# Optimization experiments

Hardware: AMD Instinct MI355X
Metric: run time of the kernel (lower is better)

Reference implementation:

```python
import jax, jax.numpy as jnp
import numpy as np
from jax import lax

DN = ('NCHW', 'OIHW', 'NCHW')

def _conv(x, k, stride):
    return lax.conv_general_dilated(x, k, (stride, stride), 'VALID', dimension_numbers=DN)

def setup_inputs() -> dict:
    key = jax.random.key(0)
    ks = jax.random.split(key, 20)
    B, E, A, D = 2048, 8, 6, 64 * 7 * 7  # batch, rm_states, actions, flat conv dim (3136)
    s = 0.05
    inp = {
        'state': jax.random.normal(ks[0], (B, 84, 84, 3), jnp.float32),
        'rm_state': jax.random.randint(ks[1], (B,), 0, E, jnp.int64),
        # conv encoder params
        'k1': jax.random.normal(ks[2], (32, 3, 8, 8), jnp.float32) * s,
        'c1': jnp.zeros((32,), jnp.float32),
        'k2': jax.random.normal(ks[3], (64, 32, 4, 4), jnp.float32) * s,
        'c2': jnp.zeros((64,), jnp.float32),
        'k3': jax.random.normal(ks[4], (64, 64, 3, 3), jnp.float32) * s,
        'c3': jnp.zeros((64,), jnp.float32),
        # stacked per-rm-state expert MLP params (E experts)
        'W1': jax.random.normal(ks[5], (E, D, 64), jnp.float32) * s,
        'B1': jnp.zeros((E, 64), jnp.float32),
        'W2': jax.random.normal(ks[6], (E, 64, 64), jnp.float32) * s,
        'B2': jnp.zeros((E, 64), jnp.float32),
        'W3': jax.random.normal(ks[7], (E, 64, 64), jnp.float32) * s,
        'B3': jnp.zeros((E, 64), jnp.float32),
        'W4': jax.random.normal(ks[8], (E, 64, 64), jnp.float32) * s,
        'B4': jnp.zeros((E, 64), jnp.float32),
        'W5': jax.random.normal(ks[9], (E, 64, 64), jnp.float32) * s,
        'B5': jnp.zeros((E, 64), jnp.float32),
        'W6': jax.random.normal(ks[10], (E, 64, A), jnp.float32) * s,
        'B6': jnp.zeros((E, A), jnp.float32),
    }
    return inp

def reference(state, rm_state, k1, c1, k2, c2, k3, c3,
              W1, B1, W2, B2, W3, B3, W4, B4, W5, B5, W6, B6):
    # NHWC -> NCHW (matches torch's view-based channel-first rearrangement intent)
    x = jnp.transpose(state, (0, 3, 1, 2))
    x = jax.nn.relu(_conv(x, k1, 4) + c1[None, :, None, None])
    x = jax.nn.relu(_conv(x, k2, 2) + c2[None, :, None, None])
    x = jax.nn.relu(_conv(x, k3, 1) + c3[None, :, None, None])
    B = x.shape[0]
    flat = x.reshape(B, -1)                              # [B, 3136]
    # batched expert MLPs: compute all experts, then gather per-sample expert output
    h = jax.nn.relu(jnp.einsum('bd,edh->ebh', flat, W1) + B1[:, None, :])  # [E,B,64]
    for W, Bb in ((W2, B2), (W3, B3), (W4, B4), (W5, B5)):
        h = jax.nn.relu(jnp.einsum('ebh,ehk->ebk', h, W) + Bb[:, None, :])
    out = jnp.einsum('ebh,eha->eba', h, W6) + B6[:, None, :]               # [E,B,A]
    return out[rm_state, jnp.arange(B)]                  # [B, A]
```

## Files before the change

### kernel.cpp

```cpp
#include <hip/hip_runtime.h>

#define BATCH 2048

typedef unsigned short u16;
typedef __attribute__((ext_vector_type(8))) short bf16x8;
typedef __attribute__((ext_vector_type(4))) float f32x4;

static __device__ __forceinline__ float b2f(u16 h) {
  union { unsigned u; float f; } x; x.u = ((unsigned)h) << 16; return x.f;
}
static __device__ __forceinline__ u16 f2b(float f) {
  union { float f; unsigned u; } x; x.f = f;
  return (u16)((x.u + 0x7fffu + ((x.u >> 16) & 1u)) >> 16);
}
static __device__ __forceinline__ void split2(float v, u16& h, u16& l) {
  h = f2b(v); l = f2b(v - b2f(h));
}
static __device__ __forceinline__ bf16x8 ld8u(const u16* p, int idx) {
  union { bf16x8 v; ushort4 u[2]; } x;
  x.u[0] = *(const ushort4*)(p + idx);
  x.u[1] = *(const ushort4*)(p + idx + 4);
  return x.v;
}

__global__ void wsplit_kernel(const float* __restrict__ k1,
                              const float* __restrict__ k2,
                              const float* __restrict__ k3,
                              u16* __restrict__ W1d, u16* __restrict__ W2d,
                              u16* __restrict__ W3d)
{
  int id = blockIdx.x * 256 + threadIdx.x;
  float v; u16 *dh, *dl;
  if (id < 8192) {
    int ky = id >> 10, oc = (id >> 5) & 31, kk = id & 31;
    if (kk < 24) {
      int kx = kk / 3, c = kk - kx * 3;
      v = k1[oc * 192 + c * 64 + ky * 8 + kx];
    } else v = 0.f;
    dh = W1d + id; dl = W1d + 8192 + id;
  } else if (id < 40960) {
    int i = id - 8192;
    int pos = i >> 11, oc = (i >> 5) & 63, cc = i & 31;
    int ky = pos >> 2, kx = pos & 3;
    v = k2[oc * 512 + cc * 16 + ky * 4 + kx];
    dh = W2d + i; dl = W2d + 32768 + i;
  } else {
    int i = id - 40960;
    int j = i & 31, oc = (i >> 5) & 63, kc = (i >> 11) & 1, pos = i >> 12;
    int ky = pos / 3, kx = pos - ky * 3;
    v = k3[oc * 576 + (kc * 32 + j) * 9 + ky * 3 + kx];
    dh = W3d + i; dl = W3d + 36864 + i;
  }
  u16 h, l; split2(v, h, l); *dh = h; *dl = l;
}

__global__ void w1split_kernel(const float* __restrict__ W1,
                               u16* __restrict__ W1s)
{
  const int bc = blockIdx.x;
  const int e = bc / 98, chunk = bc - e * 98;
  const int t = threadIdx.x;
  const float* in = W1 + (size_t)e * 200704 + chunk * 2048;
  const int c = t >> 2, kk0 = (t & 3) * 8;
  u16 h[8], l[8];
  #pragma unroll
  for (int j = 0; j < 8; ++j) {
    float v = in[(kk0 + j) * 64 + c];
    split2(v, h[j], l[j]);
  }
  ushort4 h0; h0.x = h[0]; h0.y = h[1]; h0.z = h[2]; h0.w = h[3];
  ushort4 h1; h1.x = h[4]; h1.y = h[5]; h1.z = h[6]; h1.w = h[7];
  ushort4 l0; l0.x = l[0]; l0.y = l[1]; l0.z = l[2]; l0.w = l[3];
  ushort4 l1; l1.x = l[4]; l1.y = l[5]; l1.z = l[6]; l1.w = l[7];
  size_t d = (size_t)e * 200704 + chunk * 2048 + t * 8;
  *(ushort4*)(W1s + d)     = h0;
  *(ushort4*)(W1s + d + 4) = h1;
  *(ushort4*)(W1s + 1605632 + d)     = l0;
  *(ushort4*)(W1s + 1605632 + d + 4) = l1;
}

__global__ __launch_bounds__(512, 4) void conv_fused_kernel(
    const float* __restrict__ state, const u16* __restrict__ W1d,
    const u16* __restrict__ W2d, const u16* __restrict__ W3d,
    const float* __restrict__ c1, const float* __restrict__ c2,
    const float* __restrict__ c3, u16* __restrict__ a3h,
    u16* __restrict__ a3l)
{
  __shared__ __align__(16) u16 A1h[14400], A1l[14400];
  __shared__ __align__(16) u16 SHa[5832], SHb[5832];

  const int b = blockIdx.x, t = threadIdx.x;
  const int lane = t & 63, w = t >> 6, q = lane >> 4, n = lane & 15;

  for (int i = t; i < 792; i += 512) { SHa[5040 + i] = 0; SHb[5040 + i] = 0; }

  const int nT1 = (w < 2) ? 2 : 1;
  int pt1[2], ot1[2];
  if (w < 2) { pt1[0] = 0; ot1[0] = w; pt1[1] = 4; ot1[1] = w; }
  else       { pt1[0] = 1 + ((w - 2) >> 1); ot1[0] = (w - 2) & 1;
               pt1[1] = pt1[0]; ot1[1] = ot1[0]; }

  int aoff1[2];
  #pragma unroll
  for (int i = 0; i < 2; ++i) {
    int px = pt1[i] * 16 + n;
    int py = (px * 205) >> 12, pxx = px - py * 20;
    aoff1[i] = (py * 4) * 252 + pxx * 12 + q * 8;
  }
  float c1v[2];
  #pragma unroll
  for (int j = 0; j < 2; ++j) c1v[j] = c1[ot1[j] * 16 + n];
  const int ob1 = (ot1[0] * 16 + n) * 32 + q * 8;

  for (int by = 0; by < 5; ++by) {
    __syncthreads();
    const float4* sp = (const float4*)(state + (size_t)b * 21168 + by * 4032);
    #pragma unroll
    for (int pass = 0; pass < 3; ++pass) {
      int i = t + pass * 512;
      if (i < 1260) {
        float4 v = sp[i];
        u16 h0, l0, h1, l1, h2, l2, h3, l3;
        split2(v.x, h0, l0); split2(v.y, h1, l1);
        split2(v.z, h2, l2); split2(v.w, h3, l3);
        ushort4 hh; hh.x = h0; hh.y = h1; hh.z = h2; hh.w = h3;
        ushort4 ll; ll.x = l0; ll.y = l1; ll.z = l2; ll.w = l3;
        *(ushort4*)&SHa[i * 4] = hh;
        *(ushort4*)&SHb[i * 4] = ll;
      }
    }
    __syncthreads();

    f32x4 acc1[2] = {};
    bf16x8 bhc = *(const bf16x8*)(W1d + ob1);
    bf16x8 boc = *(const bf16x8*)(W1d + 8192 + ob1);
    for (int ky = 0; ky < 8; ++ky) {
      const int kyn = (ky < 7) ? ky + 1 : 7;
      bf16x8 bhn = *(const bf16x8*)(W1d + kyn * 1024 + ob1);
      bf16x8 bon = *(const bf16x8*)(W1d + 8192 + kyn * 1024 + ob1);
      #pragma unroll
      for (int i = 0; i < 2; ++i) if (i < nT1) {
        bf16x8 ah = ld8u(SHa, aoff1[i] + ky * 252);
        bf16x8 al = ld8u(SHb, aoff1[i] + ky * 252);
        acc1[i] = __builtin_amdgcn_mfma_f32_16x16x32_bf16(ah, bhc, acc1[i], 0, 0, 0);
        acc1[i] = __builtin_amdgcn_mfma_f32_16x16x32_bf16(ah, boc, acc1[i], 0, 0, 0);
        acc1[i] = __builtin_amdgcn_mfma_f32_16x16x32_bf16(al, bhc, acc1[i], 0, 0, 0);
      }
      bhc = bhn; boc = bon;
    }
    #pragma unroll
    for (int i = 0; i < 2; ++i) if (i < nT1) {
      int oc = ot1[i] * 16 + n;
      #pragma unroll
      for (int r = 0; r < 4; ++r) {
        int px = by * 80 + pt1[i] * 16 + q * 4 + r;
        float v = fmaxf(acc1[i][r] + c1v[i], 0.f);
        u16 h, l; split2(v, h, l);
        A1h[px * 36 + oc] = h; A1l[px * 36 + oc] = l;
      }
    }
  }
  __syncthreads();

  {
    const int ot2 = w & 3, pg2 = (w >> 2) * 3;
    int aoff2[3];
    #pragma unroll
    for (int i = 0; i < 3; ++i) {
      int px = (pg2 + i) * 16 + n; if (px > 80) px = 80;
      int py = (px * 7282) >> 16, pxx = px - py * 9;
      aoff2[i] = 2 * (py * 20 + pxx) * 36 + q * 8;
    }
    const float c2v = c2[ot2 * 16 + n];
    const int ob2 = (ot2 * 16 + n) * 32 + q * 8;

    f32x4 acc2[3] = {};
    bf16x8 bhc = *(const bf16x8*)(W2d + ob2);
    bf16x8 boc = *(const bf16x8*)(W2d + 32768 + ob2);
    for (int pos = 0; pos < 16; ++pos) {
      const int posn = (pos < 15) ? pos + 1 : 15;
      bf16x8 bhn = *(const bf16x8*)(W2d + posn * 2048 + ob2);
      bf16x8 bon = *(const bf16x8*)(W2d + 32768 + posn * 2048 + ob2);
      const int o = ((pos >> 2) * 20 + (pos & 3)) * 36;
      #pragma unroll
      for (int i = 0; i < 3; ++i) {
        bf16x8 ah = ld8u(A1h, aoff2[i] + o);
        bf16x8 al = ld8u(A1l, aoff2[i] + o);
        acc2[i] = __builtin_amdgcn_mfma_f32_16x16x32_bf16(ah, bhc, acc2[i], 0, 0, 0);
        acc2[i] = __builtin_amdgcn_mfma_f32_16x16x32_bf16(ah, boc, acc2[i], 0, 0, 0);
        acc2[i] = __builtin_amdgcn_mfma_f32_16x16x32_bf16(al, bhc, acc2[i], 0, 0, 0);
      }
      bhc = bhn; boc = bon;
    }
    #pragma unroll
    for (int i = 0; i < 3; ++i) {
      int oc = ot2 * 16 + n;
      #pragma unroll
      for (int r = 0; r < 4; ++r) {
        int px = (pg2 + i) * 16 + q * 4 + r;
        if (px < 81) {
          float v = fmaxf(acc2[i][r] + c2v, 0.f);
          u16 h, l; split2(v, h, l);
          SHa[px * 72 + oc] = h; SHb[px * 72 + oc] = l;
        }
      }
    }
  }
  __syncthreads();

  {
    const int ot3 = w & 3, pg3 = (w >> 2) * 2;
    int aoff3[2];
    #pragma unroll
    for (int i = 0; i < 2; ++i) {
      int px = (pg3 + i) * 16 + n; if (px > 48) px = 48;
      int py = (px * 74) >> 9, pxx = px - py * 7;
      aoff3[i] = (py * 9 + pxx) * 72 + q * 8;
    }
    const float c3v = c3[ot3 * 16 + n];
    const int ob3 = (ot3 * 16 + n) * 32 + q * 8;

    f32x4 acc3[2] = {};
    bf16x8 bhc = *(const bf16x8*)(W3d + ob3);
    bf16x8 boc = *(const bf16x8*)(W3d + 36864 + ob3);
    for (int pk = 0; pk < 18; ++pk) {
      const int pkn = (pk < 17) ? pk + 1 : 17;
      bf16x8 bhn = *(const bf16x8*)(W3d + pkn * 2048 + ob3);
      bf16x8 bon = *(const bf16x8*)(W3d + 36864 + pkn * 2048 + ob3);
      const int pos = pk >> 1, kc = pk & 1;
      const int ky = pos / 3, kx = pos - ky * 3;
      const int o = (ky * 9 + kx) * 72 + kc * 32;
      #pragma unroll
      for (int i = 0; i < 2; ++i) {
        bf16x8 ah = *(const bf16x8*)&SHa[aoff3[i] + o];
        bf16x8 al = *(const bf16x8*)&SHb[aoff3[i] + o];
        acc3[i] = __builtin_amdgcn_mfma_f32_16x16x32_bf16(ah, bhc, acc3[i], 0, 0, 0);
        acc3[i] = __builtin_amdgcn_mfma_f32_16x16x32_bf16(ah, boc, acc3[i], 0, 0, 0);
        acc3[i] = __builtin_amdgcn_mfma_f32_16x16x32_bf16(al, bhc, acc3[i], 0, 0, 0);
      }
      bhc = bhn; boc = bon;
    }
    u16* oph = a3h + (size_t)b * 3136;
    u16* opl = a3l + (size_t)b * 3136;
    #pragma unroll
    for (int i = 0; i < 2; ++i) {
      int oc = ot3 * 16 + n;
      #pragma unroll
      for (int r = 0; r < 4; ++r) {
        int px = (pg3 + i) * 16 + q * 4 + r;
        if (px < 49) {
          float v = fmaxf(acc3[i][r] + c3v, 0.f);
          u16 h, l; split2(v, h, l);
          oph[oc * 49 + px] = h; opl[oc * 49 + px] = l;
        }
      }
    }
  }
}

__global__ void group_kernel(const void* __restrict__ rmv,
                             int* __restrict__ counts, int* __restrict__ idxb)
{
  __shared__ int lcnt[8];
  __shared__ int isI32;
  const int t = threadIdx.x;
  if (t == 0) isI32 = 0;
  if (t < 8) lcnt[t] = 0;
  __syncthreads();
  unsigned long long v = ((const unsigned long long*)rmv)[t];
  if (v >= 8ull) isI32 = 1;
  __syncthreads();
  const int i32 = isI32;
  for (int b = t; b < BATCH; b += 1024) {
    int e = i32 ? ((const int*)rmv)[b] : (int)((const long long*)rmv)[b];
    int pos = atomicAdd(&lcnt[e], 1);
    idxb[e * BATCH + pos] = b;
  }
  __syncthreads();
  if (t < 8) counts[t] = lcnt[t];
}

__global__ __launch_bounds__(512, 4) void mlp_kernel(
    const u16* __restrict__ a3h, const u16* __restrict__ a3l,
    const int* __restrict__ counts, const int* __restrict__ idxb,
    const u16* __restrict__ W1s, const float* __restrict__ B1,
    const float* __restrict__ W2, const float* __restrict__ B2,
    const float* __restrict__ W3, const float* __restrict__ B3,
    const float* __restrict__ W4, const float* __restrict__ B4,
    const float* __restrict__ W5, const float* __restrict__ B5,
    const float* __restrict__ W6, const float* __restrict__ B6,
    float* __restrict__ out)
{
  __shared__ __align__(16) float Ht0[64 * 36];
  __shared__ __align__(16) float Ht1[64 * 36];
  __shared__ __align__(16) float Wl[4096];
  __shared__ float bl[64];
  __shared__ float W6l[384];
  __shared__ float B6l[8];
  __shared__ int s_id[32];

  const int e  = blockIdx.x >> 6;
  const int tl = blockIdx.x & 63;
  const int cnt = counts[e];
  const int n0 = tl * 32;
  if (n0 >= cnt) return;
  const int m = min(32, cnt - n0);
  const int t = threadIdx.x;
  if (t < 32)  s_id[t] = idxb[e * BATCH + n0 + min(t, m - 1)];
  if (t < 384) W6l[t] = W6[e * 384 + t];
  if (t < 6)   B6l[t] = B6[e * 6 + t];
  __syncthreads();

  const int lane = t & 63, w = t >> 6, q = lane >> 4, n = lane & 15;
  const int mh = w >> 2, nt = w & 3;
  const u16* Wb = W1s + (size_t)e * 200704;
  const size_t srow = (size_t)s_id[mh * 16 + n] * 3136;
  const int aoff = q * 8;
  const int obase = (nt * 16 + n) * 32 + q * 8;

  f32x4 acc = {};
  bf16x8 ahc = *(const bf16x8*)(a3h + srow + aoff);
  bf16x8 alc = *(const bf16x8*)(a3l + srow + aoff);
  bf16x8 bhc = *(const bf16x8*)(Wb + obase);
  bf16x8 boc = *(const bf16x8*)(Wb + 1605632 + obase);
  for (int ch = 0; ch < 98; ++ch) {
    const int chn = (ch < 97) ? ch + 1 : 97;
    bf16x8 ahn = *(const bf16x8*)(a3h + srow + chn * 32 + aoff);
    bf16x8 aln = *(const bf16x8*)(a3l + srow + chn * 32 + aoff);
    bf16x8 bhn = *(const bf16x8*)(Wb + chn * 2048 + obase);
    bf16x8 bon = *(const bf16x8*)(Wb + 1605632 + chn * 2048 + obase);
    acc = __builtin_amdgcn_mfma_f32_16x16x32_bf16(ahc, bhc, acc, 0, 0, 0);
    acc = __builtin_amdgcn_mfma_f32_16x16x32_bf16(ahc, boc, acc, 0, 0, 0);
    acc = __builtin_amdgcn_mfma_f32_16x16x32_bf16(alc, bhc, acc, 0, 0, 0);
    ahc = ahn; alc = aln; bhc = bhn; boc = bon;
  }

  {
    const int c = nt * 16 + n;
    const float b1v = B1[e * 64 + c];
    #pragma unroll
    for (int rr = 0; rr < 4; ++rr)
      Ht0[c * 36 + mh * 16 + q * 4 + rr] = fmaxf(acc[rr] + b1v, 0.f);
  }

  const int r0 = t >> 4, c0 = (t & 15) * 4;
  const float* Ws[4] = {W2, W3, W4, W5};
  const float* Bs[4] = {B2, B3, B4, B5};
  float* Hc = Ht0; float* Hn = Ht1;

  for (int L = 0; L < 4; ++L) {
    __syncthreads();
    const float* We = Ws[L] + (size_t)e * 4096;
    for (int i = t; i < 1024; i += 512)
      *(float4*)&Wl[i * 4] = *(const float4*)&We[i * 4];
    if (t < 64) bl[t] = Bs[L][e * 64 + t];
    __syncthreads();

    float acc4[4] = {};
    #pragma unroll 4
    for (int kk = 0; kk < 64; ++kk) {
      float a = Hc[kk * 36 + r0];
      float4 bb = *(const float4*)&Wl[kk * 64 + c0];
      acc4[0] += a * bb.x; acc4[1] += a * bb.y;
      acc4[2] += a * bb.z; acc4[3] += a * bb.w;
    }
    __syncthreads();
    #pragma unroll
    for (int j = 0; j < 4; ++j)
      Hn[(c0 + j) * 36 + r0] = fmaxf(acc4[j] + bl[c0 + j], 0.f);
    float* tmp = Hc; Hc = Hn; Hn = tmp;
  }
  __syncthreads();

  const int r = t & 31, aa = t >> 5;
  if (aa < 6) {
    float s = 0.f;
    for (int k = 0; k < 64; ++k)
      s += Hc[k * 36 + r] * W6l[k * 6 + aa];
    if (r < m) out[s_id[r] * 6 + aa] = s + B6l[aa];
  }
}

extern "C" void kernel_launch(void* const* d_in, const int* in_sizes, int n_in,
                              void* d_out, int out_size, void* d_ws, size_t ws_size,
                              hipStream_t stream) {
  const float* state = (const float*)d_in[0];
  const void*  rm    = d_in[1];
  const float* k1 = (const float*)d_in[2];
  const float* c1 = (const float*)d_in[3];
  const float* k2 = (const float*)d_in[4];
  const float* c2 = (const float*)d_in[5];
  const float* k3 = (const float*)d_in[6];
  const float* c3 = (const float*)d_in[7];
  const float* W1 = (const float*)d_in[8];
  const float* B1 = (const float*)d_in[9];
  const float* W2 = (const float*)d_in[10];
  const float* B2 = (const float*)d_in[11];
  const float* W3 = (const float*)d_in[12];
  const float* B3 = (const float*)d_in[13];
  const float* W4 = (const float*)d_in[14];
  const float* B4 = (const float*)d_in[15];
  const float* W5 = (const float*)d_in[16];
  const float* B5 = (const float*)d_in[17];
  const float* W6 = (const float*)d_in[18];
  const float* B6 = (const float*)d_in[19];

  char* ws = (char*)d_ws;
  u16* a3h    = (u16*)(ws);
  u16* a3l    = (u16*)(ws + 12845056);
  int* counts = (int*)(ws + 25690112);
  int* idxb   = (int*)(ws + 25690144);
  u16* W1d    = (u16*)(ws + 25755680);
  u16* W2d    = (u16*)(ws + 25788448);
  u16* W3d    = (u16*)(ws + 25919520);
  u16* W1s    = (u16*)(ws + 26066976);

  wsplit_kernel<<<304, 256, 0, stream>>>(k1, k2, k3, W1d, W2d, W3d);
  w1split_kernel<<<784, 256, 0, stream>>>(W1, W1s);
  group_kernel<<<1, 1024, 0, stream>>>(rm, counts, idxb);

  conv_fused_kernel<<<2048, 512, 0, stream>>>(state, W1d, W2d, W3d,
                                              c1, c2, c3, a3h, a3l);

  mlp_kernel<<<512, 512, 0, stream>>>(a3h, a3l, counts, idxb, W1s, B1,
                                      W2, B2, W3, B3, W4, B4, W5, B5,
                                      W6, B6, (float*)d_out);
}
```

Measured before the change: 531.8 us.

## Reorder conv1 output by parity, pad LDS strides, prefetch input rows

```diff
diff --git a/kernel.cpp b/kernel.cpp
--- a/kernel.cpp
+++ b/kernel.cpp
@@ -20,6 +20,14 @@
   union { bf16x8 v; ushort4 u[2]; } x;
   x.u[0] = *(const ushort4*)(p + idx);
   x.u[1] = *(const ushort4*)(p + idx + 4);
+  return x.v;
+}
+static __device__ __forceinline__ bf16x8 ld8w(const u16* p, int idx) {
+  union { bf16x8 v; ushort2 u[4]; } x;
+  x.u[0] = *(const ushort2*)(p + idx);
+  x.u[1] = *(const ushort2*)(p + idx + 2);
+  x.u[2] = *(const ushort2*)(p + idx + 4);
+  x.u[3] = *(const ushort2*)(p + idx + 6);
   return x.v;
 }
 
@@ -86,8 +94,8 @@
     const float* __restrict__ c3, u16* __restrict__ a3h,
     u16* __restrict__ a3l)
 {
-  __shared__ __align__(16) u16 A1h[14400], A1l[14400];
-  __shared__ __align__(16) u16 SHa[5832], SHb[5832];
+  __shared__ __align__(16) u16 A1h[13600], A1l[13600];
+  __shared__ __align__(16) u16 SHa[5994], SHb[5994];
 
   const int b = blockIdx.x, t = threadIdx.x;
   const int lane = t & 63, w = t >> 6, q = lane >> 4, n = lane & 15;
@@ -112,22 +120,43 @@
   for (int j = 0; j < 2; ++j) c1v[j] = c1[ot1[j] * 16 + n];
   const int ob1 = (ot1[0] * 16 + n) * 32 + q * 8;
 
+  const float4* spB = (const float4*)(state + (size_t)b * 21168);
+  float4 rb0, rb1, rb2;
+  rb0 = spB[t];
+  if (t < 748) rb1 = spB[t + 512];
+  if (t < 236) rb2 = spB[t + 1024];
+
   for (int by = 0; by < 5; ++by) {
     __syncthreads();
-    const float4* sp = (const float4*)(state + (size_t)b * 21168 + by * 4032);
-    #pragma unroll
-    for (int pass = 0; pass < 3; ++pass) {
-      int i = t + pass * 512;
-      if (i < 1260) {
-        float4 v = sp[i];
-        u16 h0, l0, h1, l1, h2, l2, h3, l3;
-        split2(v.x, h0, l0); split2(v.y, h1, l1);
-        split2(v.z, h2, l2); split2(v.w, h3, l3);
-        ushort4 hh; hh.x = h0; hh.y = h1; hh.z = h2; hh.w = h3;
-        ushort4 ll; ll.x = l0; ll.y = l1; ll.z = l2; ll.w = l3;
-        *(ushort4*)&SHa[i * 4] = hh;
-        *(ushort4*)&SHb[i * 4] = ll;
-      }
+    {
+      float4 v = rb0;
+      u16 h0,l0,h1,l1,h2,l2,h3,l3;
+      split2(v.x,h0,l0); split2(v.y,h1,l1); split2(v.z,h2,l2); split2(v.w,h3,l3);
+      ushort4 hh; hh.x=h0; hh.y=h1; hh.z=h2; hh.w=h3;
+      ushort4 ll; ll.x=l0; ll.y=l1; ll.z=l2; ll.w=l3;
+      *(ushort4*)&SHa[t * 4] = hh; *(ushort4*)&SHb[t * 4] = ll;
+    }
+    if (t < 748) {
+      float4 v = rb1;
+      u16 h0,l0,h1,l1,h2,l2,h3,l3;
+      split2(v.x,h0,l0); split2(v.y,h1,l1); split2(v.z,h2,l2); split2(v.w,h3,l3);
+      ushort4 hh; hh.x=h0; hh.y=h1; hh.z=h2; hh.w=h3;
+      ushort4 ll; ll.x=l0; ll.y=l1; ll.z=l2; ll.w=l3;
+      *(ushort4*)&SHa[(t + 512) * 4] = hh; *(ushort4*)&SHb[(t + 512) * 4] = ll;
+    }
+    if (t < 236) {
+      float4 v = rb2;
+      u16 h0,l0,h1,l1,h2,l2,h3,l3;
+      split2(v.x,h0,l0); split2(v.y,h1,l1); split2(v.z,h2,l2); split2(v.w,h3,l3);
+      ushort4 hh; hh.x=h0; hh.y=h1; hh.z=h2; hh.w=h3;
+      ushort4 ll; ll.x=l0; ll.y=l1; ll.z=l2; ll.w=l3;
+      *(ushort4*)&SHa[(t + 1024) * 4] = hh; *(ushort4*)&SHb[(t + 1024) * 4] = ll;
+    }
+    if (by < 4) {
+      const float4* spN = spB + (by + 1) * 1008;
+      rb0 = spN[t];
+      if (t < 748) rb1 = spN[t + 512];
+      if (t < 236) rb2 = spN[t + 1024];
     }
     __syncthreads();
 
@@ -154,9 +183,11 @@
       #pragma unroll
       for (int r = 0; r < 4; ++r) {
         int px = by * 80 + pt1[i] * 16 + q * 4 + r;
+        int y = (px * 205) >> 12, x = px - y * 20;
+        int r1 = (y & 1) * 200 + (y >> 1) * 20 + (x & 1) * 10 + (x >> 1);
         float v = fmaxf(acc1[i][r] + c1v[i], 0.f);
         u16 h, l; split2(v, h, l);
-        A1h[px * 36 + oc] = h; A1l[px * 36 + oc] = l;
+        A1h[r1 * 34 + oc] = h; A1l[r1 * 34 + oc] = l;
       }
     }
   }
@@ -167,9 +198,9 @@
     int aoff2[3];
     #pragma unroll
     for (int i = 0; i < 3; ++i) {
-      int px = (pg2 + i) * 16 + n; if (px > 80) px = 80;
-      int py = (px * 7282) >> 16, pxx = px - py * 9;
-      aoff2[i] = 2 * (py * 20 + pxx) * 36 + q * 8;
+      int o = (pg2 + i) * 16 + n; if (o > 80) o = 80;
+      int oy = (o * 7282) >> 16, ox = o - oy * 9;
+      aoff2[i] = (oy * 20 + ox) * 34 + q * 8;
     }
     const float c2v = c2[ot2 * 16 + n];
     const int ob2 = (ot2 * 16 + n) * 32 + q * 8;
@@ -181,11 +212,13 @@
       const int posn = (pos < 15) ? pos + 1 : 15;
       bf16x8 bhn = *(const bf16x8*)(W2d + posn * 2048 + ob2);
       bf16x8 bon = *(const bf16x8*)(W2d + 32768 + posn * 2048 + ob2);
-      const int o = ((pos >> 2) * 20 + (pos & 3)) * 36;
+      const int ky = pos >> 2, kx = pos & 3;
+      const int o2 = ((ky & 1) * 200 + (ky >> 1) * 20 +
+                      (kx & 1) * 10 + (kx >> 1)) * 34;
       #pragma unroll
       for (int i = 0; i < 3; ++i) {
-        bf16x8 ah = ld8u(A1h, aoff2[i] + o);
-        bf16x8 al = ld8u(A1l, aoff2[i] + o);
+        bf16x8 ah = ld8w(A1h, aoff2[i] + o2);
+        bf16x8 al = ld8w(A1l, aoff2[i] + o2);
         acc2[i] = __builtin_amdgcn_mfma_f32_16x16x32_bf16(ah, bhc, acc2[i], 0, 0, 0);
         acc2[i] = __builtin_amdgcn_mfma_f32_16x16x32_bf16(ah, boc, acc2[i], 0, 0, 0);
         acc2[i] = __builtin_amdgcn_mfma_f32_16x16x32_bf16(al, bhc, acc2[i], 0, 0, 0);
@@ -201,7 +234,7 @@
         if (px < 81) {
           float v = fmaxf(acc2[i][r] + c2v, 0.f);
           u16 h, l; split2(v, h, l);
-          SHa[px * 72 + oc] = h; SHb[px * 72 + oc] = l;
+          SHa[px * 74 + oc] = h; SHb[px * 74 + oc] = l;
         }
       }
     }
@@ -215,7 +248,7 @@
     for (int i = 0; i < 2; ++i) {
       int px = (pg3 + i) * 16 + n; if (px > 48) px = 48;
       int py = (px * 74) >> 9, pxx = px - py * 7;
-      aoff3[i] = (py * 9 + pxx) * 72 + q * 8;
+      aoff3[i] = (py * 9 + pxx) * 74 + q * 8;
     }
     const float c3v = c3[ot3 * 16 + n];
     const int ob3 = (ot3 * 16 + n) * 32 + q * 8;
@@ -229,11 +262,11 @@
       bf16x8 bon = *(const bf16x8*)(W3d + 36864 + pkn * 2048 + ob3);
       const int pos = pk >> 1, kc = pk & 1;
       const int ky = pos / 3, kx = pos - ky * 3;
-      const int o = (ky * 9 + kx) * 72 + kc * 32;
+      const int o3 = (ky * 9 + kx) * 74 + kc * 32;
       #pragma unroll
       for (int i = 0; i < 2; ++i) {
-        bf16x8 ah = *(const bf16x8*)&SHa[aoff3[i] + o];
-        bf16x8 al = *(const bf16x8*)&SHb[aoff3[i] + o];
+        bf16x8 ah = ld8w(SHa, aoff3[i] + o3);
+        bf16x8 al = ld8w(SHb, aoff3[i] + o3);
         acc3[i] = __builtin_amdgcn_mfma_f32_16x16x32_bf16(ah, bhc, acc3[i], 0, 0, 0);
         acc3[i] = __builtin_amdgcn_mfma_f32_16x16x32_bf16(ah, boc, acc3[i], 0, 0, 0);
         acc3[i] = __builtin_amdgcn_mfma_f32_16x16x32_bf16(al, bhc, acc3[i], 0, 0, 0);
```

Measured after the change: 515.8 us. 1.03x faster.
